# Performance work log

Hardware: AMD Instinct MI355X
Metric: run time of the kernel (lower is better)

Reference implementation:

```python
import jax, jax.numpy as jnp
import numpy as np

N_NODES = 100000
N_EDGES = 1200000
IN_DIM = 256
HID = 64


def _spmm(rows, cols, vals, M):
    # sparse (COO) @ dense: gather source rows, scale by edge vals, scatter-add to dest
    gathered = M[cols] * vals[:, None]          # [E, d]
    return jax.ops.segment_sum(gathered, rows, num_segments=N_NODES)


def _gcn_embed(rows, cols, vals, X, W1, b1, W2, b2):
    # layer 1: SELU(A @ (X W1) + b1)
    Z = _spmm(rows, cols, vals, X @ W1) + b1
    Z = jax.nn.selu(Z)
    # layer 2: A @ (Z W2) + b2 (no activation)
    Z = _spmm(rows, cols, vals, Z @ W2) + b2
    # row-wise L2 normalize (F.normalize, p=2, dim=1)
    norm = jnp.sqrt(jnp.sum(Z * Z, axis=1, keepdims=True))
    return Z / jnp.maximum(norm, 1e-12)


def setup_inputs() -> dict:
    key = jax.random.key(0)
    ks = jax.random.split(key, 10)
    X1 = jax.random.normal(ks[0], (N_NODES, IN_DIM), dtype=jnp.float32)
    X2 = jax.random.normal(ks[1], (N_NODES, IN_DIM), dtype=jnp.float32)
    rows1 = jax.random.randint(ks[2], (N_EDGES,), 0, N_NODES, dtype=jnp.int32)
    cols1 = jax.random.randint(ks[3], (N_EDGES,), 0, N_NODES, dtype=jnp.int32)
    vals1 = jax.random.uniform(ks[4], (N_EDGES,), dtype=jnp.float32)
    rows2 = jax.random.randint(ks[5], (N_EDGES,), 0, N_NODES, dtype=jnp.int32)
    cols2 = jax.random.randint(ks[6], (N_EDGES,), 0, N_NODES, dtype=jnp.int32)
    vals2 = jax.random.uniform(ks[7], (N_EDGES,), dtype=jnp.float32)
    # Xavier-uniform weights, zero biases (reset_parameters)
    lim1 = float(np.sqrt(6.0 / (IN_DIM + HID)))
    lim2 = float(np.sqrt(6.0 / (HID + HID)))
    W1 = jax.random.uniform(ks[8], (IN_DIM, HID), dtype=jnp.float32, minval=-lim1, maxval=lim1)
    W2 = jax.random.uniform(ks[9], (HID, HID), dtype=jnp.float32, minval=-lim2, maxval=lim2)
    b1 = jnp.zeros((HID,), dtype=jnp.float32)
    b2 = jnp.zeros((HID,), dtype=jnp.float32)
    return {"X1": X1, "X2": X2, "rows1": rows1, "cols1": cols1, "vals1": vals1,
            "rows2": rows2, "cols2": cols2, "vals2": vals2,
            "W1": W1, "b1": b1, "W2": W2, "b2": b2}


def reference(X1, X2, rows1, cols1, vals1, rows2, cols2, vals2, W1, b1, W2, b2):
    Z1 = _gcn_embed(rows1, cols1, vals1, X1, W1, b1, W2, b2)
    Z2 = _gcn_embed(rows2, cols2, vals2, X2, W1, b1, W2, b2)
    return (Z1, Z2)
```

## Files before the change

kernel.cpp:

```cpp
#include <hip/hip_runtime.h>
#include <hip/hip_bf16.h>


#define RPB 512
#define EPB 4096
#define MAXB 8192

typedef __attribute__((ext_vector_type(8))) short short8;
typedef __attribute__((ext_vector_type(4))) short short4v;
typedef __attribute__((ext_vector_type(4))) float f32x4;

#define GEMM_LDS 36864
#define SCAT_LDS 52224
#define SORT_LDS 72704

__device__ __forceinline__ float selu_f(float x) {
    const float scale = 1.0507009873554805f;
    const float alpha = 1.6732632423543772f;
    return x > 0.0f ? scale * x : scale * alpha * (__expf(x) - 1.0f);
}

__device__ __forceinline__ short f2bf(float x) {
    unsigned u = __float_as_uint(x);
    u += 0x7FFF + ((u >> 16) & 1);
    return (short)(u >> 16);
}
__device__ __forceinline__ float bf2f(short h) {
    return __uint_as_float(((unsigned)(unsigned short)h) << 16);
}

__global__ void scan_a(const int* __restrict__ countsB, int* __restrict__ offsB,
                       int* __restrict__ partialsB, int N) {
    const int* counts = countsB + (size_t)blockIdx.y * N;
    int* offs = offsB + (size_t)blockIdx.y * (N + 1);
    int* partials = partialsB + (size_t)blockIdx.y * 512;
    __shared__ int sh[256];
    int tid = threadIdx.x;
    int base = blockIdx.x * 1024 + tid * 4;
    int4 c = make_int4(0, 0, 0, 0);
    if (base + 3 < N) {
        c = *(const int4*)(counts + base);
    } else {
        if (base + 0 < N) c.x = counts[base + 0];
        if (base + 1 < N) c.y = counts[base + 1];
        if (base + 2 < N) c.z = counts[base + 2];
        if (base + 3 < N) c.w = counts[base + 3];
    }
    int tsum = c.x + c.y + c.z + c.w;
    sh[tid] = tsum;
    __syncthreads();
    int val = tsum;
    for (int d = 1; d < 256; d <<= 1) {
        int t = (tid >= d) ? sh[tid - d] : 0;
        __syncthreads();
        val += t;
        sh[tid] = val;
        __syncthreads();
    }
    int excl = val - tsum;
    int4 o;
    o.x = excl; o.y = o.x + c.x; o.z = o.y + c.y; o.w = o.z + c.z;
    if (base + 3 < N) {
        *(int4*)(offs + base) = o;
    } else {
        if (base + 0 < N) offs[base + 0] = o.x;
        if (base + 1 < N) offs[base + 1] = o.y;
        if (base + 2 < N) offs[base + 2] = o.z;
        if (base + 3 < N) offs[base + 3] = o.w;
    }
    if (tid == 255) partials[blockIdx.x] = val;
}

__global__ void scan_b(int* __restrict__ partialsB, int nb) {
    int* partials = partialsB + (size_t)blockIdx.y * 512;
    __shared__ int sh[128];
    int tid = threadIdx.x;
    int v = (tid < nb) ? partials[tid] : 0;
    sh[tid] = v;
    __syncthreads();
    int val = v;
    for (int d = 1; d < 128; d <<= 1) {
        int t = (tid >= d) ? sh[tid - d] : 0;
        __syncthreads();
        val += t;
        sh[tid] = val;
        __syncthreads();
    }
    if (tid < nb) partials[tid] = val - v;
}

__global__ void scan_c(int* __restrict__ offsB, const int* __restrict__ partialsB,
                       int N, int E) {
    int* offs = offsB + (size_t)blockIdx.y * (N + 1);
    const int* partials = partialsB + (size_t)blockIdx.y * 512;
    int tid = threadIdx.x;
    int base = blockIdx.x * 1024 + tid * 4;
    int add = partials[blockIdx.x];
    if (base + 3 < N) {
        int4 o = *(int4*)(offs + base);
        o.x += add; o.y += add; o.z += add; o.w += add;
        *(int4*)(offs + base) = o;
    } else {
        for (int t = 0; t < 4; t++)
            if (base + t < N) offs[base + t] += add;
    }
    if (blockIdx.x == 0 && tid == 0) offs[N] = E;
}


__device__ __forceinline__ void role_hist(const int* __restrict__ rows,
                                          int* __restrict__ cntT,
                                          int E, int nbA, int NB, int bx,
                                          int* cnt) {
    int tid = threadIdx.x;
    cnt[tid] = 0;
    __syncthreads();
    int e0 = bx * EPB;
#pragma unroll
    for (int k = 0; k < EPB / 256; k++) {
        int e = e0 + k * 256 + tid;
        if (e < E) atomicAdd(&cnt[rows[e] >> 9], 1);
    }
    __syncthreads();
    if (tid < NB) cntT[tid * nbA + bx] = cnt[tid];
}

__device__ __forceinline__ void role_scatter(const int* __restrict__ rows,
                                             const int* __restrict__ cols,
                                             const float* __restrict__ vals,
                                             const int* __restrict__ csOffs,
                                             int2* __restrict__ ecvA,
                                             int E, int nbA, int NB, int bx,
                                             char* smem) {
    int* cnt = (int*)smem;
    int* loc = cnt + 256;
    int* gof = loc + 256;
    int* dstBase = gof + 256;
    int2* eLDS = (int2*)(dstBase + EPB);
    int tid = threadIdx.x;
    int e0 = bx * EPB;
    cnt[tid] = 0;
    __syncthreads();
#pragma unroll
    for (int k = 0; k < EPB / 256; k++) {
        int e = e0 + k * 256 + tid;
        if (e < E) atomicAdd(&cnt[rows[e] >> 9], 1);
    }
    __syncthreads();
    int my = cnt[tid];
    loc[tid] = my;
    __syncthreads();
    int val = my;
    for (int d = 1; d < 256; d <<= 1) {
        int t = (tid >= d) ? loc[tid - d] : 0;
        __syncthreads();
        val += t;
        loc[tid] = val;
        __syncthreads();
    }
    int excl = val - my;
    loc[tid] = excl;
    cnt[tid] = excl;
    gof[tid] = (tid < NB) ? csOffs[tid * nbA + bx] : 0;
    __syncthreads();
#pragma unroll
    for (int k = 0; k < EPB / 256; k++) {
        int e = e0 + k * 256 + tid;
        if (e < E) {
            int r = rows[e];
            int b = r >> 9;
            int p = atomicAdd(&cnt[b], 1);
            eLDS[p] = make_int2(((r & (RPB - 1)) << 17) | cols[e],
                                __float_as_int(vals[e]));
            dstBase[p] = gof[b] - loc[b];
        }
    }
    __syncthreads();
    int nE = min(EPB, E - e0);
    for (int j = tid; j < nE; j += 256)
        ecvA[dstBase[j] + j] = eLDS[j];
}

__device__ __forceinline__ void role_sort(const int* __restrict__ csOffs,
                                          const int2* __restrict__ ecvA,
                                          int2* __restrict__ ecv,
                                          int* __restrict__ offs,
                                          int nbA, int N, int E, int b,
                                          char* smem) {
    int* rcnt = (int*)smem;
    int* roff = rcnt + 512;
    int* rcur = roff + 512;
    int* sh   = rcur + 512;
    int2* eLDS = (int2*)(sh + 256);
    int tid = threadIdx.x;
    int bs = csOffs[b * nbA];
    int be = csOffs[(b + 1) * nbA];
    int cntE = be - bs;
    if (cntE > MAXB) cntE = MAXB;
    rcnt[tid] = 0;
    rcnt[tid + 256] = 0;
    __syncthreads();
    for (int j = tid; j < cntE; j += 256)
        atomicAdd(&rcnt[ecvA[bs + j].x >> 17], 1);
    __syncthreads();
    int a0 = rcnt[2 * tid], a1 = rcnt[2 * tid + 1];
    int ps = a0 + a1;
    sh[tid] = ps;
    __syncthreads();
    int val = ps;
    for (int d = 1; d < 256; d <<= 1) {
        int t = (tid >= d) ? sh[tid - d] : 0;
        __syncthreads();
        val += t;
        sh[tid] = val;
        __syncthreads();
    }
    int exclPair = val - ps;
    roff[2 * tid] = exclPair;
    roff[2 * tid + 1] = exclPair + a0;
    rcur[2 * tid] = exclPair;
    rcur[2 * tid + 1] = exclPair + a0;
    __syncthreads();
    int row0 = b * RPB;
    for (int t2 = tid; t2 < RPB; t2 += 256) {
        int row = row0 + t2;
        if (row <= N) offs[row] = bs + roff[t2];
    }
    if (b == 0 && tid == 0) offs[N] = E;
    for (int j = tid; j < cntE; j += 256) {
        int2 p = ecvA[bs + j];
        int pos = atomicAdd(&rcur[p.x >> 17], 1);
        if (pos < MAXB) eLDS[pos] = make_int2(p.x & 0x1FFFF, p.y);
    }
    __syncthreads();
    for (int j = tid; j < cntE; j += 256)
        ecv[bs + j] = eLDS[j];
}

__device__ __forceinline__ void role_gemm256(const float* __restrict__ A,
                                             const short* __restrict__ Wth,
                                             const short* __restrict__ Wtl,
                                             float* __restrict__ C, int M,
                                             int tile, char* smem) {
    constexpr int K = 256, NC = K / 64;
    short* Ah = (short*)smem;
    short* Al = Ah + 64 * 72;
    short* Wh = Al + 64 * 72;
    short* Wl = Wh + 64 * 72;
    int tid = threadIdx.x;
    int wave = tid >> 6, lane = tid & 63;
    int m = lane & 15, q = lane >> 4;
    int row0 = tile * 64;
    int ai = tid >> 4;
    int aj = (tid & 15) * 4;
    f32x4 acc[4] = {{0.f, 0.f, 0.f, 0.f}, {0.f, 0.f, 0.f, 0.f},
                    {0.f, 0.f, 0.f, 0.f}, {0.f, 0.f, 0.f, 0.f}};
    float4 ga[4];
#pragma unroll
    for (int v = 0; v < 4; v++) {
        int gr = row0 + v * 16 + ai;
        ga[v] = make_float4(0.f, 0.f, 0.f, 0.f);
        if (gr < M) ga[v] = *(const float4*)(A + (size_t)gr * K + aj);
    }
#pragma unroll
    for (int c = 0; c < NC; c++) {
        short4v whv[4], wlv[4];
#pragma unroll
        for (int v = 0; v < 4; v++) {
            size_t wo = (size_t)(v * 16 + ai) * K + c * 64 + aj;
            whv[v] = *(const short4v*)(Wth + wo);
            wlv[v] = *(const short4v*)(Wtl + wo);
        }
        float4 gan[4];
        if (c + 1 < NC) {
#pragma unroll
            for (int v = 0; v < 4; v++) {
                int gr = row0 + v * 16 + ai;
                gan[v] = make_float4(0.f, 0.f, 0.f, 0.f);
                if (gr < M)
                    gan[v] = *(const float4*)(A + (size_t)gr * K + (c + 1) * 64 + aj);
            }
        }
#pragma unroll
        for (int v = 0; v < 4; v++) {
            int r = v * 16 + ai;
            float f[4] = {ga[v].x, ga[v].y, ga[v].z, ga[v].w};
            short4v h, l;
#pragma unroll
            for (int j = 0; j < 4; j++) {
                short hh = f2bf(f[j]);
                h[j] = hh;
                l[j] = f2bf(f[j] - bf2f(hh));
            }
            *(short4v*)(&Ah[r * 72 + aj]) = h;
            *(short4v*)(&Al[r * 72 + aj]) = l;
        }
#pragma unroll
        for (int v = 0; v < 4; v++) {
            int n = v * 16 + ai;
            *(short4v*)(&Wh[n * 72 + aj]) = whv[v];
            *(short4v*)(&Wl[n * 72 + aj]) = wlv[v];
        }
        __syncthreads();
        int ar = (16 * wave + m) * 72;
        short8 ah0 = *(const short8*)(&Ah[ar + q * 8]);
        short8 ah1 = *(const short8*)(&Ah[ar + 32 + q * 8]);
        short8 al0 = *(const short8*)(&Al[ar + q * 8]);
        short8 al1 = *(const short8*)(&Al[ar + 32 + q * 8]);
#pragma unroll
        for (int nt = 0; nt < 4; nt++) {
            int nb = (nt * 16 + m) * 72;
            short8 bh0 = *(const short8*)(&Wh[nb + q * 8]);
            short8 bh1 = *(const short8*)(&Wh[nb + 32 + q * 8]);
            short8 bl0 = *(const short8*)(&Wl[nb + q * 8]);
            short8 bl1 = *(const short8*)(&Wl[nb + 32 + q * 8]);
            acc[nt] = __builtin_amdgcn_mfma_f32_16x16x32_bf16(ah0, bh0, acc[nt], 0, 0, 0);
            acc[nt] = __builtin_amdgcn_mfma_f32_16x16x32_bf16(al0, bh0, acc[nt], 0, 0, 0);
            acc[nt] = __builtin_amdgcn_mfma_f32_16x16x32_bf16(ah0, bl0, acc[nt], 0, 0, 0);
            acc[nt] = __builtin_amdgcn_mfma_f32_16x16x32_bf16(ah1, bh1, acc[nt], 0, 0, 0);
            acc[nt] = __builtin_amdgcn_mfma_f32_16x16x32_bf16(al1, bh1, acc[nt], 0, 0, 0);
            acc[nt] = __builtin_amdgcn_mfma_f32_16x16x32_bf16(ah1, bl1, acc[nt], 0, 0, 0);
        }
        if (c + 1 < NC) {
            __syncthreads();
#pragma unroll
            for (int v = 0; v < 4; v++) ga[v] = gan[v];
        }
    }
#pragma unroll
    for (int nt = 0; nt < 4; nt++) {
#pragma unroll
        for (int r = 0; r < 4; r++) {
            int grow = row0 + 16 * wave + q * 4 + r;
            if (grow < M) C[(size_t)grow * 64 + nt * 16 + m] = acc[nt][r];
        }
    }
}


__global__ __launch_bounds__(256) void fat_hist_gemm(
        const int* __restrict__ r0, const int* __restrict__ r1,
        int* __restrict__ cntTB, int E, int nbA, int NB, int Mcnt,
        const float* __restrict__ X1, const float* __restrict__ X2,
        const short* __restrict__ w1th, const short* __restrict__ w1tl,
        float* __restrict__ C0, float* __restrict__ C1, int Nn,
        int t0, int tcnt) {
    __shared__ __align__(16) char smem[GEMM_LDS];
    int id = blockIdx.x;
    int nCsr = 2 * nbA;
    if (id < nCsr) {
        int gph = id / nbA, bx = id % nbA;
        role_hist(gph ? r1 : r0, cntTB + (size_t)gph * Mcnt, E, nbA, NB, bx,
                  (int*)smem);
    } else {
        int gid = id - nCsr;
        int gph = gid / tcnt;
        int tile = t0 + gid - gph * tcnt;
        role_gemm256(gph ? X2 : X1, w1th, w1tl, gph ? C1 : C0, Nn, tile, smem);
    }
}

__global__ __launch_bounds__(256) void fat_scatter_gemm(
        const int* __restrict__ r0, const int* __restrict__ r1,
        const int* __restrict__ c0, const int* __restrict__ c1,
        const float* __restrict__ v0, const float* __restrict__ v1,
        const int* __restrict__ csOffsB, int2* __restrict__ ecvAB,
        int E, int nbA, int NB, int Mcnt,
        const float* __restrict__ X1, const float* __restrict__ X2,
        const short* __restrict__ w1th, const short* __restrict__ w1tl,
        float* __restrict__ C0, float* __restrict__ C1, int Nn,
        int t0, int tcnt) {
    __shared__ __align__(16) char smem[SCAT_LDS];
    int id = blockIdx.x;
    int nCsr = 2 * nbA;
    if (id < nCsr) {
        int gph = id / nbA, bx = id % nbA;
        role_scatter(gph ? r1 : r0, gph ? c1 : c0, gph ? v1 : v0,
                     csOffsB + (size_t)gph * (Mcnt + 1),
                     ecvAB + (size_t)gph * E, E, nbA, NB, bx, smem);
    } else {
        int gid = id - nCsr;
        int gph = gid / tcnt;
        int tile = t0 + gid - gph * tcnt;
        role_gemm256(gph ? X2 : X1, w1th, w1tl, gph ? C1 : C0, Nn, tile, smem);
    }
}

__global__ __launch_bounds__(256) void fat_sort_gemm(
        const int* __restrict__ csOffsB, const int2* __restrict__ ecvAB,
        int2* __restrict__ ecvB, int* __restrict__ offsB,
        int nbA, int N, int E, int Mcnt, int NB,
        const float* __restrict__ X1, const float* __restrict__ X2,
        const short* __restrict__ w1th, const short* __restrict__ w1tl,
        float* __restrict__ C0, float* __restrict__ C1, int Nn,
        int t0, int tcnt) {
    __shared__ __align__(16) char smem[SORT_LDS];
    int id = blockIdx.x;
    int nCsr = 2 * NB;
    if (id < nCsr) {
        int gph = id / NB, b = id % NB;
        role_sort(csOffsB + (size_t)gph * (Mcnt + 1),
                  ecvAB + (size_t)gph * E,
                  ecvB + (size_t)gph * E,
                  offsB + (size_t)gph * (N + 1),
                  nbA, N, E, b, smem);
    } else {
        int gid = id - nCsr;
        int gph = gid / tcnt;
        int tile = t0 + gid - gph * tcnt;
        role_gemm256(gph ? X2 : X1, w1th, w1tl, gph ? C1 : C0, Nn, tile, smem);
    }
}

__global__ void prep_w2(const float* __restrict__ W1, short* __restrict__ th1,
                        short* __restrict__ tl1,
                        const float* __restrict__ W2, short* __restrict__ th2,
                        short* __restrict__ tl2) {
    int idx = blockIdx.x * 256 + threadIdx.x;
    const int n1 = 256 * 64;
    if (idx < n1) {
        int k = idx >> 6, n = idx & 63;
        float x = W1[idx];
        short h = f2bf(x);
        short l = f2bf(x - bf2f(h));
        th1[n * 256 + k] = h;
        tl1[n * 256 + k] = l;
    } else if (idx - n1 < 64 * 64) {
        int i2 = idx - n1;
        int k = i2 >> 6, n = i2 & 63;
        float x = W2[i2];
        short h = f2bf(x);
        short l = f2bf(x - bf2f(h));
        th2[n * 64 + k] = h;
        tl2[n * 64 + k] = l;
    }
}

__device__ __forceinline__ void spmm_row4(const int* __restrict__ offs,
                                          const int2* __restrict__ ecv,
                                          const float* __restrict__ H,
                                          int row, int g, int f4,
                                          float& ax, float& ay, float& az, float& aw) {
    int s = offs[row], e = offs[row + 1];
    s = __builtin_amdgcn_readfirstlane(s);
    e = __builtin_amdgcn_readfirstlane(e);
    ax = ay = az = aw = 0.f;
    for (int i = s; i < e; i += 16) {
        int i0 = i + g, i1 = i + 4 + g, i2 = i + 8 + g, i3 = i + 12 + g;
        int2 p0 = ecv[i0 < e ? i0 : (e - 1)];
        int2 p1 = ecv[i1 < e ? i1 : (e - 1)];
        int2 p2 = ecv[i2 < e ? i2 : (e - 1)];
        int2 p3 = ecv[i3 < e ? i3 : (e - 1)];
        float v0 = (i0 < e) ? __int_as_float(p0.y) : 0.f;
        float v1 = (i1 < e) ? __int_as_float(p1.y) : 0.f;
        float v2 = (i2 < e) ? __int_as_float(p2.y) : 0.f;
        float v3 = (i3 < e) ? __int_as_float(p3.y) : 0.f;
        float4 h0 = *(const float4*)(H + (size_t)p0.x * 64 + f4);
        float4 h1 = *(const float4*)(H + (size_t)p1.x * 64 + f4);
        float4 h2 = *(const float4*)(H + (size_t)p2.x * 64 + f4);
        float4 h3 = *(const float4*)(H + (size_t)p3.x * 64 + f4);
        ax = fmaf(v0, h0.x, ax); ay = fmaf(v0, h0.y, ay);
        az = fmaf(v0, h0.z, az); aw = fmaf(v0, h0.w, aw);
        ax = fmaf(v1, h1.x, ax); ay = fmaf(v1, h1.y, ay);
        az = fmaf(v1, h1.z, az); aw = fmaf(v1, h1.w, aw);
        ax = fmaf(v2, h2.x, ax); ay = fmaf(v2, h2.y, ay);
        az = fmaf(v2, h2.z, az); aw = fmaf(v2, h2.w, aw);
        ax = fmaf(v3, h3.x, ax); ay = fmaf(v3, h3.y, ay);
        az = fmaf(v3, h3.z, az); aw = fmaf(v3, h3.w, aw);
    }
#pragma unroll
    for (int d = 16; d <= 32; d <<= 1) {
        ax += __shfl_xor(ax, d, 64);
        ay += __shfl_xor(ay, d, 64);
        az += __shfl_xor(az, d, 64);
        aw += __shfl_xor(aw, d, 64);
    }
}

__global__ __launch_bounds__(256) void spmm_selu_w2(const int* __restrict__ offsB,
                                                    const int2* __restrict__ ecvB,
                                                    const float* __restrict__ HB,
                                                    const float* __restrict__ bias,
                                                    const short* __restrict__ w2th,
                                                    const short* __restrict__ w2tl,
                                                    float* __restrict__ outB,
                                                    int N, int E) {
    int gph = blockIdx.y;
    const int* offs = offsB + (size_t)gph * (N + 1);
    const int2* ecv = ecvB + (size_t)gph * E;
    const float* H = HB + (size_t)gph * N * 64;
    float* out = outB + (size_t)gph * N * 64;
    __shared__ short Zh[16 * 72], Zl[16 * 72];
    int tid = threadIdx.x, wave = tid >> 6, lane = tid & 63;
    int g = lane >> 4, f4 = (lane & 15) * 4;
    int rbase = blockIdx.x * 16;
    float4 b = *(const float4*)(bias + f4);
#pragma unroll
    for (int rr = 0; rr < 4; rr++) {
        int lr = wave * 4 + rr;
        int row = rbase + lr;
        if (row < N) {
            float ax, ay, az, aw;
            spmm_row4(offs, ecv, H, row, g, f4, ax, ay, az, aw);
            if (g == 0) {
                float zx = selu_f(ax + b.x);
                float zy = selu_f(ay + b.y);
                float zz = selu_f(az + b.z);
                float zw = selu_f(aw + b.w);
                short4v h, l;
                h.x = f2bf(zx); l.x = f2bf(zx - bf2f(h.x));
                h.y = f2bf(zy); l.y = f2bf(zy - bf2f(h.y));
                h.z = f2bf(zz); l.z = f2bf(zz - bf2f(h.z));
                h.w = f2bf(zw); l.w = f2bf(zw - bf2f(h.w));
                *(short4v*)(&Zh[lr * 72 + f4]) = h;
                *(short4v*)(&Zl[lr * 72 + f4]) = l;
            }
        } else if (g == 0) {
            short4v zv = {0, 0, 0, 0};
            *(short4v*)(&Zh[lr * 72 + f4]) = zv;
            *(short4v*)(&Zl[lr * 72 + f4]) = zv;
        }
    }
    __syncthreads();
    int m_ = lane & 15, q = lane >> 4;
    int ar = m_ * 72;
    short8 ah0 = *(const short8*)(&Zh[ar + q * 8]);
    short8 ah1 = *(const short8*)(&Zh[ar + 32 + q * 8]);
    short8 al0 = *(const short8*)(&Zl[ar + q * 8]);
    short8 al1 = *(const short8*)(&Zl[ar + 32 + q * 8]);
    const short* bhp = w2th + (size_t)(wave * 16 + m_) * 64;
    const short* blp = w2tl + (size_t)(wave * 16 + m_) * 64;
    short8 bh0 = *(const short8*)(bhp + q * 8);
    short8 bh1 = *(const short8*)(bhp + 32 + q * 8);
    short8 bl0 = *(const short8*)(blp + q * 8);
    short8 bl1 = *(const short8*)(blp + 32 + q * 8);
    f32x4 acc = {0.f, 0.f, 0.f, 0.f};
    acc = __builtin_amdgcn_mfma_f32_16x16x32_bf16(ah0, bh0, acc, 0, 0, 0);
    acc = __builtin_amdgcn_mfma_f32_16x16x32_bf16(al0, bh0, acc, 0, 0, 0);
    acc = __builtin_amdgcn_mfma_f32_16x16x32_bf16(ah0, bl0, acc, 0, 0, 0);
    acc = __builtin_amdgcn_mfma_f32_16x16x32_bf16(ah1, bh1, acc, 0, 0, 0);
    acc = __builtin_amdgcn_mfma_f32_16x16x32_bf16(al1, bh1, acc, 0, 0, 0);
    acc = __builtin_amdgcn_mfma_f32_16x16x32_bf16(ah1, bl1, acc, 0, 0, 0);
#pragma unroll
    for (int r = 0; r < 4; r++) {
        int grow = rbase + q * 4 + r;
        if (grow < N) out[(size_t)grow * 64 + wave * 16 + m_] = acc[r];
    }
}

__global__ __launch_bounds__(256) void spmm_norm(const int* __restrict__ offsB,
                                                 const int2* __restrict__ ecvB,
                                                 const float* __restrict__ HB,
                                                 const float* __restrict__ bias,
                                                 float* __restrict__ outB,
                                                 int N, int E) {
    int gph = blockIdx.y;
    const int* offs = offsB + (size_t)gph * (N + 1);
    const int2* ecv = ecvB + (size_t)gph * E;
    const float* H = HB + (size_t)gph * N * 64;
    float* out = outB + (size_t)gph * N * 64;
    int row = blockIdx.x * 4 + (threadIdx.x >> 6);
    if (row >= N) return;
    int lane = threadIdx.x & 63;
    int g = lane >> 4, f4 = (lane & 15) * 4;
    float ax, ay, az, aw;
    spmm_row4(offs, ecv, H, row, g, f4, ax, ay, az, aw);
    float4 b = *(const float4*)(bias + f4);
    float zx = ax + b.x, zy = ay + b.y, zz = az + b.z, zw = aw + b.w;
    float s2 = zx * zx + zy * zy + zz * zz + zw * zw;
#pragma unroll
    for (int d = 1; d <= 8; d <<= 1) s2 += __shfl_xor(s2, d, 64);
    float inv = 1.0f / fmaxf(sqrtf(s2), 1e-12f);
    if (g == 0) {
        float4 o;
        o.x = zx * inv; o.y = zy * inv; o.z = zz * inv; o.w = zw * inv;
        *(float4*)(out + (size_t)row * 64 + f4) = o;
    }
}

extern "C" void kernel_launch(void* const* d_in, const int* in_sizes, int n_in,
                              void* d_out, int out_size, void* d_ws, size_t ws_size,
                              hipStream_t stream) {
    const int IN_DIM = 256, HID = 64;
    const int N = in_sizes[0] / IN_DIM;
    const int E = in_sizes[2];

    const float* X1 = (const float*)d_in[0];
    const float* X2 = (const float*)d_in[1];
    const int*   r0 = (const int*)d_in[2];
    const int*   c0 = (const int*)d_in[3];
    const float* v0 = (const float*)d_in[4];
    const int*   r1 = (const int*)d_in[5];
    const int*   c1 = (const int*)d_in[6];
    const float* v1 = (const float*)d_in[7];
    const float* W1 = (const float*)d_in[8];
    const float* b1 = (const float*)d_in[9];
    const float* W2 = (const float*)d_in[10];
    const float* b2 = (const float*)d_in[11];
    float* out = (float*)d_out;

    const int NB  = (N + RPB - 1) / RPB;
    const int nbA = (E + EPB - 1) / EPB;
    const int M   = NB * nbA;
    const int nbScanM = (M + 1023) / 1024;
    const int nbGemm = (N + 63) / 64;
    const int nbRow  = (N + 3) / 4;
    const int nbFuse = (N + 15) / 16;

    const int T1 = nbGemm / 10;
    const int T2 = (nbGemm * 45) / 100;
    const int T3 = nbGemm - T1 - T2;

    auto align16 = [](char* p) { return (char*)(((uintptr_t)p + 15) & ~(uintptr_t)15); };
    char* w = (char*)d_ws;
    float* bufA   = (float*)w; w += (size_t)2 * N * HID * sizeof(float);
    float* bufB   = (float*)w; w += (size_t)2 * N * HID * sizeof(float);
    w = align16(w);
    int2*  ecv    = (int2*)w;  w += (size_t)2 * E * sizeof(int2);
    w = align16(w);
    int2*  ecvA   = (int2*)w;  w += (size_t)2 * E * sizeof(int2);
    w = align16(w);
    int*   cntT   = (int*)w;   w += (size_t)2 * M * sizeof(int);
    w = align16(w);
    int*   csOffs = (int*)w;   w += (size_t)2 * (M + 1) * sizeof(int);
    w = align16(w);
    int*   offs   = (int*)w;   w += (size_t)2 * (N + 1) * sizeof(int);
    w = align16(w);
    int*   partials = (int*)w; w += 2 * 512 * sizeof(int);
    w = align16(w);
    short* w1th = (short*)w;   w += (size_t)64 * IN_DIM * sizeof(short);
    short* w1tl = (short*)w;   w += (size_t)64 * IN_DIM * sizeof(short);
    short* w2th = (short*)w;   w += (size_t)64 * HID * sizeof(short);
    short* w2tl = (short*)w;   w += (size_t)64 * HID * sizeof(short);
    float* bufA1 = bufA + (size_t)N * HID;

    prep_w2<<<(IN_DIM * 64 + HID * 64 + 255) / 256, 256, 0, stream>>>(
        W1, w1th, w1tl, W2, w2th, w2tl);

    fat_hist_gemm<<<2 * nbA + 2 * T1, 256, 0, stream>>>(
        r0, r1, cntT, E, nbA, NB, M,
        X1, X2, w1th, w1tl, bufA, bufA1, N, 0, T1);
    scan_a<<<dim3(nbScanM, 2), 256, 0, stream>>>(cntT, csOffs, partials, M);
    scan_b<<<dim3(1, 2), 128, 0, stream>>>(partials, nbScanM);
    scan_c<<<dim3(nbScanM, 2), 256, 0, stream>>>(csOffs, partials, M, E);
    fat_scatter_gemm<<<2 * nbA + 2 * T2, 256, 0, stream>>>(
        r0, r1, c0, c1, v0, v1, csOffs, ecvA, E, nbA, NB, M,
        X1, X2, w1th, w1tl, bufA, bufA1, N, T1, T2);
    fat_sort_gemm<<<2 * NB + 2 * T3, 256, 0, stream>>>(
        csOffs, ecvA, ecv, offs, nbA, N, E, M, NB,
        X1, X2, w1th, w1tl, bufA, bufA1, N, T1 + T2, T3);

    spmm_selu_w2<<<dim3(nbFuse, 2), 256, 0, stream>>>(offs, ecv, bufA, b1,
                                                      w2th, w2tl, bufB, N, E);
    spmm_norm<<<dim3(nbRow, 2), 256, 0, stream>>>(offs, ecv, bufB, b2, out, N, E);
}
```

Before: 504.5 us.

## Build CSR with global per-row atomic histogram and direct atomic scatter

Replaces the two-level bucketed counting sort (per-block bucket histograms, bucket scatter, then per-bucket row sort in LDS) with a direct per-row global atomic histogram, an exclusive scan over rows, and an atomic-cursor scatter straight into the final CSR edge array. This drops the intermediate edge buffer, the sort kernel and its extra read/write pass over all edges. Counter zeroing is folded into the weight-prep kernel, and the layer-1 GEMM tiles are re-split across the two remaining fused launches. In exchange it relies on many global atomics with return values and uncoalesced random 8-byte writes. Edge order within a row becomes nondeterministic, so floating-point summation order can vary between runs.

New measurement: 668.8 us. +32.6%, slower.

```diff
diff --git a/kernel.cpp b/kernel.cpp
--- a/kernel.cpp
+++ b/kernel.cpp
@@ -2,17 +2,12 @@
 #include <hip/hip_bf16.h>
 
 
-#define RPB 512
 #define EPB 4096
-#define MAXB 8192
+#define GEMM_LDS 36864
 
 typedef __attribute__((ext_vector_type(8))) short short8;
 typedef __attribute__((ext_vector_type(4))) short short4v;
 typedef __attribute__((ext_vector_type(4))) float f32x4;
-
-#define GEMM_LDS 36864
-#define SCAT_LDS 52224
-#define SORT_LDS 72704
 
 __device__ __forceinline__ float selu_f(float x) {
     const float scale = 1.0507009873554805f;
@@ -89,9 +84,10 @@
     if (tid < nb) partials[tid] = val - v;
 }
 
-__global__ void scan_c(int* __restrict__ offsB, const int* __restrict__ partialsB,
-                       int N, int E) {
+__global__ void scan_c(int* __restrict__ offsB, int* __restrict__ curB,
+                       const int* __restrict__ partialsB, int N, int E) {
     int* offs = offsB + (size_t)blockIdx.y * (N + 1);
+    int* cur  = curB  + (size_t)blockIdx.y * N;
     const int* partials = partialsB + (size_t)blockIdx.y * 512;
     int tid = threadIdx.x;
     int base = blockIdx.x * 1024 + tid * 4;
@@ -100,141 +96,94 @@
         int4 o = *(int4*)(offs + base);
         o.x += add; o.y += add; o.z += add; o.w += add;
         *(int4*)(offs + base) = o;
+        *(int4*)(cur + base) = o;
     } else {
         for (int t = 0; t < 4; t++)
-            if (base + t < N) offs[base + t] += add;
+            if (base + t < N) {
+                int v = offs[base + t] + add;
+                offs[base + t] = v;
+                cur[base + t] = v;
+            }
     }
     if (blockIdx.x == 0 && tid == 0) offs[N] = E;
 }
 
+__global__ void prep_zero(const float* __restrict__ W1, short* __restrict__ th1,
+                          short* __restrict__ tl1,
+                          const float* __restrict__ W2, short* __restrict__ th2,
+                          short* __restrict__ tl2,
+                          int* __restrict__ counts2, int n2) {
+    int idx = blockIdx.x * 256 + threadIdx.x;
+    const int n1 = 256 * 64;
+    if (idx < n1) {
+        int k = idx >> 6, n = idx & 63;
+        float x = W1[idx];
+        short h = f2bf(x);
+        short l = f2bf(x - bf2f(h));
+        th1[n * 256 + k] = h;
+        tl1[n * 256 + k] = l;
+    } else if (idx - n1 < 64 * 64) {
+        int i2 = idx - n1;
+        int k = i2 >> 6, n = i2 & 63;
+        float x = W2[i2];
+        short h = f2bf(x);
+        short l = f2bf(x - bf2f(h));
+        th2[n * 64 + k] = h;
+        tl2[n * 64 + k] = l;
+    }
+    for (int i = idx; i < n2; i += gridDim.x * 256) counts2[i] = 0;
+}
+
 
 __device__ __forceinline__ void role_hist(const int* __restrict__ rows,
-                                          int* __restrict__ cntT,
-                                          int E, int nbA, int NB, int bx,
-                                          int* cnt) {
+                                          int* __restrict__ cnt,
+                                          int E, int bx) {
     int tid = threadIdx.x;
-    cnt[tid] = 0;
-    __syncthreads();
     int e0 = bx * EPB;
 #pragma unroll
-    for (int k = 0; k < EPB / 256; k++) {
-        int e = e0 + k * 256 + tid;
-        if (e < E) atomicAdd(&cnt[rows[e] >> 9], 1);
-    }
-    __syncthreads();
-    if (tid < NB) cntT[tid * nbA + bx] = cnt[tid];
+    for (int k = 0; k < EPB / 1024; k++) {
+        int e = e0 + (k * 256 + tid) * 4;
+        if (e + 3 < E) {
+            int4 r4 = *(const int4*)(rows + e);
+            atomicAdd(&cnt[r4.x], 1);
+            atomicAdd(&cnt[r4.y], 1);
+            atomicAdd(&cnt[r4.z], 1);
+            atomicAdd(&cnt[r4.w], 1);
+        } else {
+            for (int t = 0; t < 4; t++)
+                if (e + t < E) atomicAdd(&cnt[rows[e + t]], 1);
+        }
+    }
 }
 
 __device__ __forceinline__ void role_scatter(const int* __restrict__ rows,
                                              const int* __restrict__ cols,
                                              const float* __restrict__ vals,
-                                             const int* __restrict__ csOffs,
-                                             int2* __restrict__ ecvA,
-                                             int E, int nbA, int NB, int bx,
-                                             char* smem) {
-    int* cnt = (int*)smem;
-    int* loc = cnt + 256;
-    int* gof = loc + 256;
-    int* dstBase = gof + 256;
-    int2* eLDS = (int2*)(dstBase + EPB);
+                                             int* __restrict__ cur,
+                                             int2* __restrict__ ecv,
+                                             int E, int bx) {
     int tid = threadIdx.x;
     int e0 = bx * EPB;
-    cnt[tid] = 0;
-    __syncthreads();
-#pragma unroll
-    for (int k = 0; k < EPB / 256; k++) {
-        int e = e0 + k * 256 + tid;
-        if (e < E) atomicAdd(&cnt[rows[e] >> 9], 1);
-    }
-    __syncthreads();
-    int my = cnt[tid];
-    loc[tid] = my;
-    __syncthreads();
-    int val = my;
-    for (int d = 1; d < 256; d <<= 1) {
-        int t = (tid >= d) ? loc[tid - d] : 0;
-        __syncthreads();
-        val += t;
-        loc[tid] = val;
-        __syncthreads();
-    }
-    int excl = val - my;
-    loc[tid] = excl;
-    cnt[tid] = excl;
-    gof[tid] = (tid < NB) ? csOffs[tid * nbA + bx] : 0;
-    __syncthreads();
-#pragma unroll
-    for (int k = 0; k < EPB / 256; k++) {
-        int e = e0 + k * 256 + tid;
-        if (e < E) {
-            int r = rows[e];
-            int b = r >> 9;
-            int p = atomicAdd(&cnt[b], 1);
-            eLDS[p] = make_int2(((r & (RPB - 1)) << 17) | cols[e],
-                                __float_as_int(vals[e]));
-            dstBase[p] = gof[b] - loc[b];
-        }
-    }
-    __syncthreads();
-    int nE = min(EPB, E - e0);
-    for (int j = tid; j < nE; j += 256)
-        ecvA[dstBase[j] + j] = eLDS[j];
-}
-
-__device__ __forceinline__ void role_sort(const int* __restrict__ csOffs,
-                                          const int2* __restrict__ ecvA,
-                                          int2* __restrict__ ecv,
-                                          int* __restrict__ offs,
-                                          int nbA, int N, int E, int b,
-                                          char* smem) {
-    int* rcnt = (int*)smem;
-    int* roff = rcnt + 512;
-    int* rcur = roff + 512;
-    int* sh   = rcur + 512;
-    int2* eLDS = (int2*)(sh + 256);
-    int tid = threadIdx.x;
-    int bs = csOffs[b * nbA];
-    int be = csOffs[(b + 1) * nbA];
-    int cntE = be - bs;
-    if (cntE > MAXB) cntE = MAXB;
-    rcnt[tid] = 0;
-    rcnt[tid + 256] = 0;
-    __syncthreads();
-    for (int j = tid; j < cntE; j += 256)
-        atomicAdd(&rcnt[ecvA[bs + j].x >> 17], 1);
-    __syncthreads();
-    int a0 = rcnt[2 * tid], a1 = rcnt[2 * tid + 1];
-    int ps = a0 + a1;
-    sh[tid] = ps;
-    __syncthreads();
-    int val = ps;
-    for (int d = 1; d < 256; d <<= 1) {
-        int t = (tid >= d) ? sh[tid - d] : 0;
-        __syncthreads();
-        val += t;
-        sh[tid] = val;
-        __syncthreads();
-    }
-    int exclPair = val - ps;
-    roff[2 * tid] = exclPair;
-    roff[2 * tid + 1] = exclPair + a0;
-    rcur[2 * tid] = exclPair;
-    rcur[2 * tid + 1] = exclPair + a0;
-    __syncthreads();
-    int row0 = b * RPB;
-    for (int t2 = tid; t2 < RPB; t2 += 256) {
-        int row = row0 + t2;
-        if (row <= N) offs[row] = bs + roff[t2];
-    }
-    if (b == 0 && tid == 0) offs[N] = E;
-    for (int j = tid; j < cntE; j += 256) {
-        int2 p = ecvA[bs + j];
-        int pos = atomicAdd(&rcur[p.x >> 17], 1);
-        if (pos < MAXB) eLDS[pos] = make_int2(p.x & 0x1FFFF, p.y);
-    }
-    __syncthreads();
-    for (int j = tid; j < cntE; j += 256)
-        ecv[bs + j] = eLDS[j];
+#pragma unroll
+    for (int k = 0; k < EPB / 1024; k++) {
+        int e = e0 + (k * 256 + tid) * 4;
+        if (e + 3 < E) {
+            int4 r4 = *(const int4*)(rows + e);
+            int4 c4 = *(const int4*)(cols + e);
+            float4 v4 = *(const float4*)(vals + e);
+            int p;
+            p = atomicAdd(&cur[r4.x], 1); ecv[p] = make_int2(c4.x, __float_as_int(v4.x));
+            p = atomicAdd(&cur[r4.y], 1); ecv[p] = make_int2(c4.y, __float_as_int(v4.y));
+            p = atomicAdd(&cur[r4.z], 1); ecv[p] = make_int2(c4.z, __float_as_int(v4.z));
+            p = atomicAdd(&cur[r4.w], 1); ecv[p] = make_int2(c4.w, __float_as_int(v4.w));
+        } else {
+            for (int t = 0; t < 4; t++)
+                if (e + t < E) {
+                    int p = atomicAdd(&cur[rows[e + t]], 1);
+                    ecv[p] = make_int2(cols[e + t], __float_as_int(vals[e + t]));
+                }
+        }
+    }
 }
 
 __device__ __forceinline__ void role_gemm256(const float* __restrict__ A,
@@ -340,23 +289,22 @@
 
 __global__ __launch_bounds__(256) void fat_hist_gemm(
         const int* __restrict__ r0, const int* __restrict__ r1,
-        int* __restrict__ cntTB, int E, int nbA, int NB, int Mcnt,
+        int* __restrict__ countsB, int E, int nbH,
         const float* __restrict__ X1, const float* __restrict__ X2,
         const short* __restrict__ w1th, const short* __restrict__ w1tl,
-        float* __restrict__ C0, float* __restrict__ C1, int Nn,
+        float* __restrict__ C0, float* __restrict__ C1, int N,
         int t0, int tcnt) {
     __shared__ __align__(16) char smem[GEMM_LDS];
     int id = blockIdx.x;
-    int nCsr = 2 * nbA;
+    int nCsr = 2 * nbH;
     if (id < nCsr) {
-        int gph = id / nbA, bx = id % nbA;
-        role_hist(gph ? r1 : r0, cntTB + (size_t)gph * Mcnt, E, nbA, NB, bx,
-                  (int*)smem);
+        int g = id / nbH, bx = id % nbH;
+        role_hist(g ? r1 : r0, countsB + (size_t)g * N, E, bx);
     } else {
         int gid = id - nCsr;
-        int gph = gid / tcnt;
-        int tile = t0 + gid - gph * tcnt;
-        role_gemm256(gph ? X2 : X1, w1th, w1tl, gph ? C1 : C0, Nn, tile, smem);
+        int g = gid / tcnt;
+        int tile = t0 + gid - g * tcnt;
+        role_gemm256(g ? X2 : X1, w1th, w1tl, g ? C1 : C0, N, tile, smem);
     }
 }
 
@@ -364,75 +312,23 @@
         const int* __restrict__ r0, const int* __restrict__ r1,
         const int* __restrict__ c0, const int* __restrict__ c1,
         const float* __restrict__ v0, const float* __restrict__ v1,
-        const int* __restrict__ csOffsB, int2* __restrict__ ecvAB,
-        int E, int nbA, int NB, int Mcnt,
+        int* __restrict__ curB, int2* __restrict__ ecvB, int E, int nbH,
         const float* __restrict__ X1, const float* __restrict__ X2,
         const short* __restrict__ w1th, const short* __restrict__ w1tl,
-        float* __restrict__ C0, float* __restrict__ C1, int Nn,
+        float* __restrict__ C0, float* __restrict__ C1, int N,
         int t0, int tcnt) {
-    __shared__ __align__(16) char smem[SCAT_LDS];
+    __shared__ __align__(16) char smem[GEMM_LDS];
     int id = blockIdx.x;
-    int nCsr = 2 * nbA;
+    int nCsr = 2 * nbH;
     if (id < nCsr) {
-        int gph = id / nbA, bx = id % nbA;
-        role_scatter(gph ? r1 : r0, gph ? c1 : c0, gph ? v1 : v0,
-                     csOffsB + (size_t)gph * (Mcnt + 1),
-                     ecvAB + (size_t)gph * E, E, nbA, NB, bx, smem);
+        int g = id / nbH, bx = id % nbH;
+        role_scatter(g ? r1 : r0, g ? c1 : c0, g ? v1 : v0,
+                     curB + (size_t)g * N, ecvB + (size_t)g * E, E, bx);
     } else {
         int gid = id - nCsr;
-        int gph = gid / tcnt;
-        int tile = t0 + gid - gph * tcnt;
-        role_gemm256(gph ? X2 : X1, w1th, w1tl, gph ? C1 : C0, Nn, tile, smem);
-    }
-}
-
-__global__ __launch_bounds__(256) void fat_sort_gemm(
-        const int* __restrict__ csOffsB, const int2* __restrict__ ecvAB,
-        int2* __restrict__ ecvB, int* __restrict__ offsB,
-        int nbA, int N, int E, int Mcnt, int NB,
-        const float* __restrict__ X1, const float* __restrict__ X2,
-        const short* __restrict__ w1th, const short* __restrict__ w1tl,
-        float* __restrict__ C0, float* __restrict__ C1, int Nn,
-        int t0, int tcnt) {
-    __shared__ __align__(16) char smem[SORT_LDS];
-    int id = blockIdx.x;
-    int nCsr = 2 * NB;
-    if (id < nCsr) {
-        int gph = id / NB, b = id % NB;
-        role_sort(csOffsB + (size_t)gph * (Mcnt + 1),
-                  ecvAB + (size_t)gph * E,
-                  ecvB + (size_t)gph * E,
-                  offsB + (size_t)gph * (N + 1),
-                  nbA, N, E, b, smem);
-    } else {
-        int gid = id - nCsr;
-        int gph = gid / tcnt;
-        int tile = t0 + gid - gph * tcnt;
-        role_gemm256(gph ? X2 : X1, w1th, w1tl, gph ? C1 : C0, Nn, tile, smem);
-    }
-}
-
-__global__ void prep_w2(const float* __restrict__ W1, short* __restrict__ th1,
-                        short* __restrict__ tl1,
-                        const float* __restrict__ W2, short* __restrict__ th2,
-                        short* __restrict__ tl2) {
-    int idx = blockIdx.x * 256 + threadIdx.x;
-    const int n1 = 256 * 64;
-    if (idx < n1) {
-        int k = idx >> 6, n = idx & 63;
-        float x = W1[idx];
-        short h = f2bf(x);
-        short l = f2bf(x - bf2f(h));
-        th1[n * 256 + k] = h;
-        tl1[n * 256 + k] = l;
-    } else if (idx - n1 < 64 * 64) {
-        int i2 = idx - n1;
-        int k = i2 >> 6, n = i2 & 63;
-        float x = W2[i2];
-        short h = f2bf(x);
-        short l = f2bf(x - bf2f(h));
-        th2[n * 64 + k] = h;
-        tl2[n * 64 + k] = l;
+        int g = gid / tcnt;
+        int tile = t0 + gid - g * tcnt;
+        role_gemm256(g ? X2 : X1, w1th, w1tl, g ? C1 : C0, N, tile, smem);
     }
 }
 
@@ -599,17 +495,14 @@
     const float* b2 = (const float*)d_in[11];
     float* out = (float*)d_out;
 
-    const int NB  = (N + RPB - 1) / RPB;
-    const int nbA = (E + EPB - 1) / EPB;
-    const int M   = NB * nbA;
-    const int nbScanM = (M + 1023) / 1024;
+    const int nbH = (E + EPB - 1) / EPB;
+    const int nbScanN = (N + 1023) / 1024;
     const int nbGemm = (N + 63) / 64;
     const int nbRow  = (N + 3) / 4;
     const int nbFuse = (N + 15) / 16;
 
-    const int T1 = nbGemm / 10;
-    const int T2 = (nbGemm * 45) / 100;
-    const int T3 = nbGemm - T1 - T2;
+    const int Ta = (nbGemm * 3) / 5;
+    const int Tb = nbGemm - Ta;
 
     auto align16 = [](char* p) { return (char*)(((uintptr_t)p + 15) & ~(uintptr_t)15); };
     char* w = (char*)d_ws;
@@ -618,13 +511,11 @@
     w = align16(w);
     int2*  ecv    = (int2*)w;  w += (size_t)2 * E * sizeof(int2);
     w = align16(w);
-    int2*  ecvA   = (int2*)w;  w += (size_t)2 * E * sizeof(int2);
-    w = align16(w);
-    int*   cntT   = (int*)w;   w += (size_t)2 * M * sizeof(int);
-    w = align16(w);
-    int*   csOffs = (int*)w;   w += (size_t)2 * (M + 1) * sizeof(int);
+    int*   counts = (int*)w;   w += (size_t)2 * N * sizeof(int);
     w = align16(w);
     int*   offs   = (int*)w;   w += (size_t)2 * (N + 1) * sizeof(int);
+    w = align16(w);
+    int*   cur    = (int*)w;   w += (size_t)2 * N * sizeof(int);
     w = align16(w);
     int*   partials = (int*)w; w += 2 * 512 * sizeof(int);
     w = align16(w);
@@ -634,21 +525,20 @@
     short* w2tl = (short*)w;   w += (size_t)64 * HID * sizeof(short);
     float* bufA1 = bufA + (size_t)N * HID;
 
-    prep_w2<<<(IN_DIM * 64 + HID * 64 + 255) / 256, 256, 0, stream>>>(
-        W1, w1th, w1tl, W2, w2th, w2tl);
-
-    fat_hist_gemm<<<2 * nbA + 2 * T1, 256, 0, stream>>>(
-        r0, r1, cntT, E, nbA, NB, M,
-        X1, X2, w1th, w1tl, bufA, bufA1, N, 0, T1);
-    scan_a<<<dim3(nbScanM, 2), 256, 0, stream>>>(cntT, csOffs, partials, M);
-    scan_b<<<dim3(1, 2), 128, 0, stream>>>(partials, nbScanM);
-    scan_c<<<dim3(nbScanM, 2), 256, 0, stream>>>(csOffs, partials, M, E);
-    fat_scatter_gemm<<<2 * nbA + 2 * T2, 256, 0, stream>>>(
-        r0, r1, c0, c1, v0, v1, csOffs, ecvA, E, nbA, NB, M,
-        X1, X2, w1th, w1tl, bufA, bufA1, N, T1, T2);
-    fat_sort_gemm<<<2 * NB + 2 * T3, 256, 0, stream>>>(
-        csOffs, ecvA, ecv, offs, nbA, N, E, M, NB,
-        X1, X2, w1th, w1tl, bufA, bufA1, N, T1 + T2, T3);
+    prep_zero<<<400, 256, 0, stream>>>(W1, w1th, w1tl, W2, w2th, w2tl,
+                                       counts, 2 * N);
+
+    fat_hist_gemm<<<2 * nbH + 2 * Ta, 256, 0, stream>>>(
+        r0, r1, counts, E, nbH,
+        X1, X2, w1th, w1tl, bufA, bufA1, N, 0, Ta);
+
+    scan_a<<<dim3(nbScanN, 2), 256, 0, stream>>>(counts, offs, partials, N);
+    scan_b<<<dim3(1, 2), 128, 0, stream>>>(partials, nbScanN);
+    scan_c<<<dim3(nbScanN, 2), 256, 0, stream>>>(offs, cur, partials, N, E);
+
+    fat_scatter_gemm<<<2 * nbH + 2 * Tb, 256, 0, stream>>>(
+        r0, r1, c0, c1, v0, v1, cur, ecv, E, nbH,
+        X1, X2, w1th, w1tl, bufA, bufA1, N, Ta, Tb);
 
     spmm_selu_w2<<<dim3(nbFuse, 2), 256, 0, stream>>>(offs, ecv, bufA, b1,
                                                       w2th, w2tl, bufB, N, E);
```
